# Kernel tuning notes

Hardware: AMD Instinct MI355X
Metric: run time of the kernel (lower is better)

Reference implementation:

```python
import jax, jax.numpy as jnp
import numpy as np
from jax import lax

EPS = 1e-5
IC = 32  # inter_channels

def bn(x, g, b, m, v):
    sh = (1, -1, 1, 1)
    return (x - m.reshape(sh)) * (g.reshape(sh) * lax.rsqrt(v.reshape(sh) + EPS)) + b.reshape(sh)

def prelu(x, a):
    return jnp.where(x >= 0, x, a * x)

def conv1x1(x, w):  # x: [B,C,H,W], w: [O,C]
    return jnp.einsum('bchw,oc->bohw', x, w)

def dconv(x, w, d):  # 3x3 dilated conv, same padding
    return lax.conv_general_dilated(x, w, (1, 1), [(d, d), (d, d)], rhs_dilation=(d, d),
                                    dimension_numbers=('NCHW', 'OIHW', 'NCHW'))

def glca_forward(feature, q_w, q_gamma, q_beta, q_mean, q_var, q_alpha,
                 k_w, k_gamma, k_beta, k_mean, k_var, k_alpha,
                 v_w, v_gamma, v_beta, v_mean, v_var, v_alpha,
                 d1_w, d1_gamma, d1_beta, d1_mean, d1_var,
                 d2_w, d2_gamma, d2_beta, d2_mean, d2_var,
                 d3_w, d3_gamma, d3_beta, d3_mean, d3_var,
                 o_w, o_gamma, o_beta, o_mean, o_var, o_alpha):
    B, C, H, W = feature.shape
    q = prelu(bn(conv1x1(feature, q_w), q_gamma, q_beta, q_mean, q_var), q_alpha)  # [B,IC,H,W]
    k = prelu(bn(conv1x1(feature, k_w), k_gamma, k_beta, k_mean, k_var), k_alpha)
    val = prelu(bn(conv1x1(feature, v_w), v_gamma, v_beta, v_mean, v_var), v_alpha)
    qr = q.transpose(0, 3, 2, 1).reshape(B * W, H, IC)   # [BW,H,IC]
    kr = k.transpose(0, 3, 1, 2).reshape(B * W, IC, H)   # [BW,IC,H]
    att = jax.nn.softmax(jnp.matmul(qr, kr), axis=-1)    # [BW,H,H]
    branches = []
    for w, g, b, m, var, d in ((d1_w, d1_gamma, d1_beta, d1_mean, d1_var, 1),
                               (d2_w, d2_gamma, d2_beta, d2_mean, d2_var, 3),
                               (d3_w, d3_gamma, d3_beta, d3_mean, d3_var, 5)):
        t = jax.nn.relu(bn(dconv(val, w, d), g, b, m, var))          # [B,IC,H,W]
        # faithful to source: permute(0,3,1,2) then raw view to [BW,H,IC]
        t = t.transpose(0, 3, 1, 2).reshape(B * W, H, IC)
        branches.append(jnp.matmul(att, t))                          # [BW,H,IC]
    # faithful to source: cat along dim 0, then raw view(B,W,H,-1)
    res = jnp.concatenate(branches, axis=0).reshape(B, W, H, 3 * IC)
    res = res.transpose(0, 3, 2, 1)                                  # [B,3*IC,H,W]
    out = prelu(bn(conv1x1(res, o_w), o_gamma, o_beta, o_mean, o_var) + feature, o_alpha)
    return out

def setup_inputs() -> dict:
    B, C, H, W = 8, 256, 160, 160
    key = jax.random.key(0)
    ks = iter(jax.random.split(key, 48))
    d = {}
    d['feature'] = jax.random.normal(next(ks), (B, C, H, W), jnp.float32)
    for p in ('q', 'k', 'v'):
        d[p + '_w'] = jax.random.normal(next(ks), (IC, C), jnp.float32) * 0.05
        d[p + '_gamma'] = jax.random.uniform(next(ks), (IC,), jnp.float32, 0.5, 1.5)
        d[p + '_beta'] = jax.random.normal(next(ks), (IC,), jnp.float32) * 0.1
        d[p + '_mean'] = jax.random.normal(next(ks), (IC,), jnp.float32) * 0.1
        d[p + '_var'] = jax.random.uniform(next(ks), (IC,), jnp.float32, 0.5, 1.5)
        d[p + '_alpha'] = jnp.full((1,), 0.25, jnp.float32)
    for p in ('d1', 'd2', 'd3'):
        d[p + '_w'] = jax.random.normal(next(ks), (IC, IC, 3, 3), jnp.float32) * 0.05
        d[p + '_gamma'] = jax.random.uniform(next(ks), (IC,), jnp.float32, 0.5, 1.5)
        d[p + '_beta'] = jax.random.normal(next(ks), (IC,), jnp.float32) * 0.1
        d[p + '_mean'] = jax.random.normal(next(ks), (IC,), jnp.float32) * 0.1
        d[p + '_var'] = jax.random.uniform(next(ks), (IC,), jnp.float32, 0.5, 1.5)
    d['o_w'] = jax.random.normal(next(ks), (C, 3 * IC), jnp.float32) * 0.05
    d['o_gamma'] = jax.random.uniform(next(ks), (C,), jnp.float32, 0.5, 1.5)
    d['o_beta'] = jax.random.normal(next(ks), (C,), jnp.float32) * 0.1
    d['o_mean'] = jax.random.normal(next(ks), (C,), jnp.float32) * 0.1
    d['o_var'] = jax.random.uniform(next(ks), (C,), jnp.float32, 0.5, 1.5)
    d['o_alpha'] = jnp.full((1,), 0.25, jnp.float32)
    return d

def reference(feature, q_w, q_gamma, q_beta, q_mean, q_var, q_alpha,
              k_w, k_gamma, k_beta, k_mean, k_var, k_alpha,
              v_w, v_gamma, v_beta, v_mean, v_var, v_alpha,
              d1_w, d1_gamma, d1_beta, d1_mean, d1_var,
              d2_w, d2_gamma, d2_beta, d2_mean, d2_var,
              d3_w, d3_gamma, d3_beta, d3_mean, d3_var,
              o_w, o_gamma, o_beta, o_mean, o_var, o_alpha):
    return glca_forward(feature, q_w, q_gamma, q_beta, q_mean, q_var, q_alpha,
                        k_w, k_gamma, k_beta, k_mean, k_var, k_alpha,
                        v_w, v_gamma, v_beta, v_mean, v_var, v_alpha,
                        d1_w, d1_gamma, d1_beta, d1_mean, d1_var,
                        d2_w, d2_gamma, d2_beta, d2_mean, d2_var,
                        d3_w, d3_gamma, d3_beta, d3_mean, d3_var,
                        o_w, o_gamma, o_beta, o_mean, o_var, o_alpha)
```

## Files before the change

kernel.cpp:

```cpp
#include <hip/hip_runtime.h>

constexpr int Hh = 160, Ww = 160, Bb = 8, Cc = 256, ICn = 32;
constexpr int HWn = Hh * Ww;
constexpr float EPSf = 1e-5f;

constexpr int P_WQH  = 0;
constexpr int P_WQL  = 12288;
constexpr int P_QKVB = 24576;
constexpr int P_QKVA = 24672;
constexpr int P_DWB  = 24768;
constexpr int P_DB   = 52416;
constexpr int P_OWB  = 52512;
constexpr int P_OB   = 77088;
constexpr int P_OA   = 77344;
constexpr int PLANE  = Bb * ICn * HWn;
constexpr int OFF_Q  = 77824;
constexpr int OFF_K  = OFF_Q + PLANE;
constexpr int OFF_V  = OFF_Q + 2 * PLANE;
constexpr int OFF_T  = OFF_Q + 3 * PLANE;
constexpr int OFF_TPF= OFF_T + (3 * PLANE) / 2;
constexpr int OFF_CAT= OFF_Q + 6 * PLANE;

typedef unsigned short u16;
typedef short bf16x8 __attribute__((ext_vector_type(8)));
typedef float f32x4  __attribute__((ext_vector_type(4)));

__device__ __forceinline__ unsigned f2b(float x) {
    unsigned u = __float_as_uint(x);
    return (u + 0x7FFFu + ((u >> 16) & 1u)) >> 16;
}
__device__ __forceinline__ float b2f(unsigned b) { return __uint_as_float(b << 16); }

struct InPtrs { const float* p[40]; };

__global__ void k_prep(InPtrs in, float* __restrict__ ws) {
    int idx = blockIdx.x * 256 + threadIdx.x;
    if (idx < 24576) {
        int oc = idx >> 8, c = idx & 255;
        int z = oc >> 5, o = oc & 31;
        const float* wz = in.p[1 + 6 * z];
        float s = in.p[2 + 6 * z][o] * rsqrtf(in.p[5 + 6 * z][o] + EPSf);
        float wf = wz[o * 256 + c] * s;
        unsigned hi = f2b(wf);
        unsigned lo = f2b(wf - b2f(hi));
        ((u16*)(ws + P_WQH))[oc * 256 + c] = (u16)hi;
        ((u16*)(ws + P_WQL))[oc * 256 + c] = (u16)lo;
    } else if (idx < 24672) {
        int oc = idx - 24576; int z = oc >> 5, o = oc & 31;
        float s = in.p[2 + 6 * z][o] * rsqrtf(in.p[5 + 6 * z][o] + EPSf);
        ws[P_QKVB + oc] = in.p[3 + 6 * z][o] - in.p[4 + 6 * z][o] * s;
    } else if (idx < 24768) {
        int oc = idx - 24672; int z = oc >> 5;
        ws[P_QKVA + oc] = in.p[6 + 6 * z][0];
    } else if (idx < 52416) {
        int j = idx - 24768;
        int d = j / 9216, r2 = j % 9216;
        int oc = r2 & 31; int tmp = r2 >> 5;
        int kx = tmp % 3; tmp /= 3; int ky = tmp % 3; int ic2 = tmp / 3;
        const float* wd = in.p[19 + 5 * d];
        float s = in.p[20 + 5 * d][oc] * rsqrtf(in.p[23 + 5 * d][oc] + EPSf);
        float wf = wd[((oc * 32 + ic2) * 3 + ky) * 3 + kx] * s;
        ((u16*)(ws + P_DWB))[((d * 9 + ky * 3 + kx) * 32 + oc) * 32 + ic2] = (u16)f2b(wf);
    } else if (idx < 52512) {
        int j = idx - 52416; int d = j >> 5, oc = j & 31;
        float s = in.p[20 + 5 * d][oc] * rsqrtf(in.p[23 + 5 * d][oc] + EPSf);
        ws[P_DB + j] = in.p[21 + 5 * d][oc] - in.p[22 + 5 * d][oc] * s;
    } else if (idx < 77088) {
        int j2 = idx - 52512; int c = j2 / 96;
        float s = in.p[35][c] * rsqrtf(in.p[38][c] + EPSf);
        ((u16*)(ws + P_OWB))[j2] = (u16)f2b(in.p[34][j2] * s);
    } else if (idx < 77344) {
        int c = idx - 77088;
        float s = in.p[35][c] * rsqrtf(in.p[38][c] + EPSf);
        ws[P_OB + c] = in.p[36][c] - in.p[37][c] * s;
    } else if (idx == 77344) {
        ws[P_OA] = in.p[39][0];
    }
}

__global__ __launch_bounds__(64) void k_vpad(float* __restrict__ ws) {
    u16* Vt = (u16*)(ws + OFF_V);
    size_t base = (size_t)blockIdx.x * 176 * 32;
    int t = threadIdx.x;
    int off = (t < 32) ? t * 8 : (168 * 32 + (t - 32) * 8);
    uint4 z = {0u, 0u, 0u, 0u};
    *(uint4*)(Vt + base + off) = z;
}

__global__ __launch_bounds__(256) void k_qkv(const float* __restrict__ feat,
                                             float* __restrict__ ws) {
    __shared__ float FS[64 * 132];
    const int tid = threadIdx.x;
    const int wv = tid >> 6, l = tid & 63;
    const int g = l >> 4, c15 = l & 15;
    const int n0 = blockIdx.x * 128;
    const int b = n0 / HWn, hw0 = n0 % HWn;
    const float* fbase = feat + (size_t)b * Cc * HWn + hw0;
    const u16* __restrict__ WQH = (const u16*)(ws + P_WQH);
    const u16* __restrict__ WQL = (const u16*)(ws + P_WQL);

    f32x4 acc[6][2];
    f32x4 z4 = {0.f, 0.f, 0.f, 0.f};
#pragma unroll
    for (int mt = 0; mt < 6; mt++) { acc[mt][0] = z4; acc[mt][1] = z4; }

    for (int kc = 0; kc < 4; kc++) {
        __syncthreads();
#pragma unroll
        for (int i = 0; i < 8; i++) {
            int f = tid + i * 256;
            int row = f >> 5, col4 = f & 31;
            float4 v = *(const float4*)(fbase + (size_t)(kc * 64 + row) * HWn + col4 * 4);
            *(float4*)(&FS[row * 132 + col4 * 4]) = v;
        }
        __syncthreads();
#pragma unroll
        for (int ks = 0; ks < 2; ks++) {
            bf16x8 bh[2], bl[2];
#pragma unroll
            for (int ntl = 0; ntl < 2; ntl++) {
                int pos = (wv * 2 + ntl) * 16 + c15;
                unsigned hw_[4], lw_[4];
#pragma unroll
                for (int v2 = 0; v2 < 4; v2++) {
                    float x0 = FS[(ks * 32 + g * 8 + 2 * v2) * 132 + pos];
                    float x1 = FS[(ks * 32 + g * 8 + 2 * v2 + 1) * 132 + pos];
                    unsigned h0 = f2b(x0), h1 = f2b(x1);
                    unsigned l0 = f2b(x0 - b2f(h0)), l1 = f2b(x1 - b2f(h1));
                    hw_[v2] = h0 | (h1 << 16);
                    lw_[v2] = l0 | (l1 << 16);
                }
                uint4 hv = {hw_[0], hw_[1], hw_[2], hw_[3]};
                uint4 lv = {lw_[0], lw_[1], lw_[2], lw_[3]};
                bh[ntl] = *(bf16x8*)&hv;
                bl[ntl] = *(bf16x8*)&lv;
            }
#pragma unroll
            for (int mt = 0; mt < 6; mt++) {
                int arow = (16 * mt + c15) * 256 + kc * 64 + ks * 32 + g * 8;
                bf16x8 ah = *(const bf16x8*)(WQH + arow);
                bf16x8 al = *(const bf16x8*)(WQL + arow);
#pragma unroll
                for (int ntl = 0; ntl < 2; ntl++) {
                    acc[mt][ntl] = __builtin_amdgcn_mfma_f32_16x16x32_bf16(ah, bh[ntl], acc[mt][ntl], 0, 0, 0);
                    acc[mt][ntl] = __builtin_amdgcn_mfma_f32_16x16x32_bf16(ah, bl[ntl], acc[mt][ntl], 0, 0, 0);
                    acc[mt][ntl] = __builtin_amdgcn_mfma_f32_16x16x32_bf16(al, bh[ntl], acc[mt][ntl], 0, 0, 0);
                }
            }
        }
    }

    u16* vt = (u16*)(ws + OFF_V);
#pragma unroll
    for (int mt = 0; mt < 6; mt++)
#pragma unroll
        for (int ntl = 0; ntl < 2; ntl++) {
            int pos = hw0 + (wv * 2 + ntl) * 16 + c15;
            if (mt < 4) {
#pragma unroll
                for (int jr = 0; jr < 4; jr++) {
                    int oc = 16 * mt + 4 * g + jr;
                    float bb = ws[P_QKVB + oc];
                    float aa = ws[P_QKVA + oc];
                    float y = acc[mt][ntl][jr] + bb;
                    y = y >= 0.f ? y : aa * y;
                    int z = oc >> 5, o = oc & 31;
                    ws[OFF_Q + (size_t)z * PLANE + ((size_t)b * ICn + o) * HWn + pos] = y;
                }
            } else {
                int h = pos / 160, w2 = pos % 160;
                unsigned r[2];
#pragma unroll
                for (int p = 0; p < 2; p++) {
                    int oc = 16 * mt + 4 * g + 2 * p;
                    float y0 = acc[mt][ntl][2 * p]     + ws[P_QKVB + oc];
                    float y1 = acc[mt][ntl][2 * p + 1] + ws[P_QKVB + oc + 1];
                    float a0 = ws[P_QKVA + oc], a1 = ws[P_QKVA + oc + 1];
                    y0 = y0 >= 0.f ? y0 : a0 * y0;
                    y1 = y1 >= 0.f ? y1 : a1 * y1;
                    r[p] = f2b(y0) | (f2b(y1) << 16);
                }
                size_t a = ((size_t)(b * 160 + h) * 176 + w2 + 8) * 32 + (mt - 4) * 16 + 4 * g;
                uint2 dd; dd.x = r[0]; dd.y = r[1];
                *(uint2*)(vt + a) = dd;
            }
        }
}

__global__ __launch_bounds__(256) void k_dconv(float* __restrict__ ws) {
    const int tid = threadIdx.x;
    const int wv = tid >> 6, l = tid & 63;
    const int g = l >> 4, c15 = l & 15;
    const int b = blockIdx.y;
    const int d = blockIdx.z;
    const int dil = 1 + 2 * d;
    const int h0 = blockIdx.x * 2;
    const u16* __restrict__ WB = (const u16*)(ws + P_DWB) + d * 9 * 32 * 32;
    bf16x8 wb[9][2];
#pragma unroll
    for (int tap = 0; tap < 9; tap++)
#pragma unroll
        for (int n = 0; n < 2; n++)
            wb[tap][n] = *(const bf16x8*)(WB + ((size_t)tap * 32 + n * 16 + c15) * 32 + g * 8);
    const u16* __restrict__ Vt = (const u16*)(ws + OFF_V) + (size_t)b * 160 * 176 * 32;
    const float bias0 = ws[P_DB + d * 32 + c15];
    const float bias1 = ws[P_DB + d * 32 + 16 + c15];
    u16* __restrict__ tp = (u16*)(ws + OFF_TPF) + (size_t)(d * Bb + b) * ICn * HWn;
    f32x4 z4 = {0.f, 0.f, 0.f, 0.f};

    for (int t5 = 0; t5 < 5; t5++) {
        int t = wv * 5 + t5;
        int h = h0 + (t >= 10);
        int w0 = (t % 10) * 16;
        f32x4 acc0 = z4, acc1 = z4;
#pragma unroll
        for (int ky = 0; ky < 3; ky++) {
            int hh = h + dil * (ky - 1);
            if ((unsigned)hh >= 160u) continue;
            const u16* row = Vt + (size_t)hh * 176 * 32;
#pragma unroll
            for (int kx = 0; kx < 3; kx++) {
                int wbase = w0 + dil * (kx - 1) + 8;
                bf16x8 av = *(const bf16x8*)(row + (size_t)(wbase + c15) * 32 + g * 8);
                acc0 = __builtin_amdgcn_mfma_f32_16x16x32_bf16(av, wb[ky * 3 + kx][0], acc0, 0, 0, 0);
                acc1 = __builtin_amdgcn_mfma_f32_16x16x32_bf16(av, wb[ky * 3 + kx][1], acc1, 0, 0, 0);
            }
        }
        size_t pixb = (size_t)h * 160 + w0 + 4 * g;
        uint2 o0, o1;
        o0.x = f2b(fmaxf(acc0[0] + bias0, 0.f)) | (f2b(fmaxf(acc0[1] + bias0, 0.f)) << 16);
        o0.y = f2b(fmaxf(acc0[2] + bias0, 0.f)) | (f2b(fmaxf(acc0[3] + bias0, 0.f)) << 16);
        o1.x = f2b(fmaxf(acc1[0] + bias1, 0.f)) | (f2b(fmaxf(acc1[1] + bias1, 0.f)) << 16);
        o1.y = f2b(fmaxf(acc1[2] + bias1, 0.f)) | (f2b(fmaxf(acc1[3] + bias1, 0.f)) << 16);
        *(uint2*)(tp + (size_t)c15 * HWn + pixb) = o0;
        *(uint2*)(tp + (size_t)(16 + c15) * HWn + pixb) = o1;
    }
}

__global__ __launch_bounds__(256) void k_tfrag(float* __restrict__ ws) {
    __shared__ u16 fr[4][5120];
    const int tid = threadIdx.x;
    const int wq = blockIdx.x;
    const int b  = blockIdx.y;
    const int d  = blockIdx.z;
    const int w0 = wq * 4;
    const u16* __restrict__ tp = (const u16*)(ws + OFF_TPF) + (size_t)(d * Bb + b) * ICn * HWn;
    for (int i = tid; i < 5120; i += 256) {
        int ic = i / 160, h = i % 160;
        uint2 v = *(const uint2*)(tp + (size_t)ic * HWn + h * Ww + w0);
        fr[0][i] = (u16)(v.x & 0xFFFFu);
        fr[1][i] = (u16)(v.x >> 16);
        fr[2][i] = (u16)(v.y & 0xFFFFu);
        fr[3][i] = (u16)(v.y >> 16);
    }
    __syncthreads();
    u16* __restrict__ tf = (u16*)(ws + OFF_T);
#pragma unroll
    for (int it = 0; it < 10; it++) {
        int W = tid + it * 256;
        int s = W / 640, word = W % 640;
        int slot = word >> 6, lane = word & 63;
        int jc = (lane & 15) | ((slot / 5) << 4);
        int h2b = ((slot % 5) << 5) | (((lane >> 4) & 3) << 3);
        unsigned r[4];
#pragma unroll
        for (int p = 0; p < 4; p++) {
            int f0 = (h2b + 2 * p) * 32 + jc;
            unsigned lo = fr[s][f0];
            unsigned hi = fr[s][f0 + 32];
            r[p] = lo | (hi << 16);
        }
        uint4 o4 = {r[0], r[1], r[2], r[3]};
        *(uint4*)(tf + ((size_t)d * 1280 + b * 160 + w0 + s) * 5120 + word * 8) = o4;
    }
}

__device__ __forceinline__ void stage_qk_hilo(const float* __restrict__ g,
                                              char* hi_buf, char* lo_buf, int tid) {
#pragma unroll
    for (int ss = 0; ss < 2; ss++) {
        int s = tid + ss * 320;
        int l = s & 63, rt = s >> 6;
        int h = 16 * rt + (l & 15);
        int icb = (l >> 4) * 8;
        const float* gp = g + (size_t)icb * HWn + h * Ww;
        unsigned hb[8], lb[8];
#pragma unroll
        for (int v = 0; v < 8; v++) {
            float x = gp[(size_t)v * HWn];
            hb[v] = f2b(x);
            lb[v] = f2b(x - b2f(hb[v]));
        }
        uint4 hv = {hb[0] | (hb[1] << 16), hb[2] | (hb[3] << 16),
                    hb[4] | (hb[5] << 16), hb[6] | (hb[7] << 16)};
        uint4 lv = {lb[0] | (lb[1] << 16), lb[2] | (lb[3] << 16),
                    lb[4] | (lb[5] << 16), lb[6] | (lb[7] << 16)};
        *(uint4*)(hi_buf + s * 16) = hv;
        *(uint4*)(lo_buf + s * 16) = lv;
    }
}

__global__ __launch_bounds__(320) void k_att(float* __restrict__ ws) {
    extern __shared__ char smem[];
    char* q_hi = smem;
    char* q_lo = smem + 10240;
    char* k_hi = smem + 20480;
    char* k_lo = smem + 30720;
    char* Sb   = smem;
    const int tid = threadIdx.x;
    const int bid = blockIdx.x;
    const int r8 = bid & 7, qq = bid >> 3;
    const int b = qq / 20;
    const int w = r8 * 20 + (qq % 20);
    const int bw = b * Ww + w;
    const int wv = tid >> 6;
    const int l  = tid & 63;
    const int g  = l >> 4;
    const int c  = l & 15;

    const float* qg = ws + OFF_Q + (size_t)b * ICn * HWn + w;
    const float* kg = ws + OFF_K + (size_t)b * ICn * HWn + w;
    stage_qk_hilo(qg, q_hi, q_lo, tid);
    stage_qk_hilo(kg, k_hi, k_lo, tid);
    __syncthreads();

    bf16x8 bq[2][2];
#pragma unroll
    for (int ct = 0; ct < 2; ct++) {
        int tau = 2 * wv + ct;
        bq[ct][0] = *(bf16x8*)(q_hi + (tau * 64 + l) * 16);
        bq[ct][1] = *(bf16x8*)(q_lo + (tau * 64 + l) * 16);
    }
    f32x4 acc[10][2];
    f32x4 z4 = {0.f, 0.f, 0.f, 0.f};
#pragma unroll
    for (int rt = 0; rt < 10; rt++) { acc[rt][0] = z4; acc[rt][1] = z4; }
#pragma unroll
    for (int rt = 0; rt < 10; rt++) {
        bf16x8 ah = *(bf16x8*)(k_hi + (rt * 64 + l) * 16);
        bf16x8 al = *(bf16x8*)(k_lo + (rt * 64 + l) * 16);
#pragma unroll
        for (int ct = 0; ct < 2; ct++) {
            acc[rt][ct] = __builtin_amdgcn_mfma_f32_16x16x32_bf16(ah, bq[ct][0], acc[rt][ct], 0, 0, 0);
            acc[rt][ct] = __builtin_amdgcn_mfma_f32_16x16x32_bf16(ah, bq[ct][1], acc[rt][ct], 0, 0, 0);
            acc[rt][ct] = __builtin_amdgcn_mfma_f32_16x16x32_bf16(al, bq[ct][0], acc[rt][ct], 0, 0, 0);
        }
    }
    __syncthreads();

    float mx[2] = {-3.4e38f, -3.4e38f};
#pragma unroll
    for (int rt = 0; rt < 10; rt++)
#pragma unroll
        for (int ct = 0; ct < 2; ct++)
#pragma unroll
            for (int j = 0; j < 4; j++) mx[ct] = fmaxf(mx[ct], acc[rt][ct][j]);
#pragma unroll
    for (int ct = 0; ct < 2; ct++) {
        mx[ct] = fmaxf(mx[ct], __shfl_xor(mx[ct], 16));
        mx[ct] = fmaxf(mx[ct], __shfl_xor(mx[ct], 32));
    }
    float sm[2] = {0.f, 0.f};
#pragma unroll
    for (int rt = 0; rt < 10; rt++)
#pragma unroll
        for (int ct = 0; ct < 2; ct++)
#pragma unroll
            for (int j = 0; j < 4; j++) {
                float e = __expf(acc[rt][ct][j] - mx[ct]);
                acc[rt][ct][j] = e;
                sm[ct] += e;
            }
#pragma unroll
    for (int ct = 0; ct < 2; ct++) {
        sm[ct] += __shfl_xor(sm[ct], 16);
        sm[ct] += __shfl_xor(sm[ct], 32);
    }
    float inv[2] = {1.f / sm[0], 1.f / sm[1]};

#pragma unroll
    for (int rt = 0; rt < 10; rt++) {
#pragma unroll
        for (int ct = 0; ct < 2; ct++) {
            float p0 = acc[rt][ct][0] * inv[ct];
            float p1 = acc[rt][ct][1] * inv[ct];
            float p2 = acc[rt][ct][2] * inv[ct];
            float p3 = acc[rt][ct][3] * inv[ct];
            unsigned d0 = f2b(p0) | (f2b(p1) << 16);
            unsigned d1 = f2b(p2) | (f2b(p3) << 16);
            int Lf = c + 16 * (2 * (rt & 1) + (g >> 1));
            char* dst = Sb + (((wv * 2 + ct) * 5 + (rt >> 1)) * 64 + Lf) * 16 + 8 * (g & 1);
            uint2 dd; dd.x = d0; dd.y = d1;
            *(uint2*)dst = dd;
        }
    }
    __syncthreads();

    const u16* tf = (const u16*)(ws + OFF_T);
    u16* catb = (u16*)(ws + OFF_CAT);
    for (int d = 0; d < 3; d++) {
        const u16* tfd = tf + ((size_t)d * (Bb * Ww) + bw) * 5120;
        f32x4 po[2][2];
        po[0][0] = z4; po[0][1] = z4; po[1][0] = z4; po[1][1] = z4;
#pragma unroll
        for (int ks = 0; ks < 5; ks++) {
            bf16x8 a0 = *(const bf16x8*)(tfd + ((0 * 5 + ks) * 64 + l) * 8);
            bf16x8 a1 = *(const bf16x8*)(tfd + ((1 * 5 + ks) * 64 + l) * 8);
            bf16x8 s0 = *(bf16x8*)(Sb + (((wv * 2 + 0) * 5 + ks) * 64 + l) * 16);
            bf16x8 s1 = *(bf16x8*)(Sb + (((wv * 2 + 1) * 5 + ks) * 64 + l) * 16);
            po[0][0] = __builtin_amdgcn_mfma_f32_16x16x32_bf16(a0, s0, po[0][0], 0, 0, 0);
            po[0][1] = __builtin_amdgcn_mfma_f32_16x16x32_bf16(a0, s1, po[0][1], 0, 0, 0);
            po[1][0] = __builtin_amdgcn_mfma_f32_16x16x32_bf16(a1, s0, po[1][0], 0, 0, 0);
            po[1][1] = __builtin_amdgcn_mfma_f32_16x16x32_bf16(a1, s1, po[1][1], 0, 0, 0);
        }
#pragma unroll
        for (int jt = 0; jt < 2; jt++)
#pragma unroll
            for (int ct = 0; ct < 2; ct++) {
                int h1 = 32 * wv + 16 * ct + c;
                size_t idx = (size_t)d * PLANE + (size_t)bw * 5120 + h1 * 32 + 16 * jt + 4 * g;
                f32x4 v = po[jt][ct];
                uint2 dd;
                dd.x = f2b(v[0]) | (f2b(v[1]) << 16);
                dd.y = f2b(v[2]) | (f2b(v[3]) << 16);
                *(uint2*)(catb + idx) = dd;
            }
    }
}

__global__ __launch_bounds__(256) void k_out(const float* __restrict__ feat,
                                             const float* __restrict__ ws,
                                             float* __restrict__ out) {
    __shared__ u16 Bs[12288];
    const int tid = threadIdx.x;
    const int wv = tid >> 6, l = tid & 63;
    const int g = l >> 4, c15 = l & 15;
    const int n0 = blockIdx.x * 128;
    const int b = n0 / HWn, hw0 = n0 % HWn;
    const u16* __restrict__ CATb = (const u16*)(ws + OFF_CAT);
    const u16* __restrict__ OWB = (const u16*)(ws + P_OWB);

#pragma unroll
    for (int ss = 0; ss < 6; ss++) {
        int s = tid + ss * 256;
        int sl = s & 63, si = s >> 6;
        int p = (si & 7) * 16 + (sl & 15);
        int hw = hw0 + p;
        int h = hw / Ww, w2 = hw % Ww;
        int j = (si >> 3) * 32 + (sl >> 4) * 8;
        size_t flat = ((size_t)(b * Ww + w2) * Hh + h) * 96 + j;
        *(uint4*)(&Bs[(si * 64 + sl) * 8]) = *(const uint4*)(CATb + flat);
    }
    bf16x8 af[4][3];
#pragma unroll
    for (int mt = 0; mt < 4; mt++)
#pragma unroll
        for (int ks = 0; ks < 3; ks++)
            af[mt][ks] = *(const bf16x8*)(OWB + (wv * 64 + mt * 16 + c15) * 96 + ks * 32 + g * 8);
    __syncthreads();
    const float alpha = ws[P_OA];

    f32x4 z4 = {0.f, 0.f, 0.f, 0.f};
#pragma unroll
    for (int np = 0; np < 2; np++) {
        f32x4 acc[4][4];
#pragma unroll
        for (int mt = 0; mt < 4; mt++)
#pragma unroll
            for (int ntl = 0; ntl < 4; ntl++) acc[mt][ntl] = z4;
#pragma unroll
        for (int ks = 0; ks < 3; ks++) {
            bf16x8 bf_[4];
#pragma unroll
            for (int ntl = 0; ntl < 4; ntl++)
                bf_[ntl] = *(const bf16x8*)(&Bs[((ks * 8 + np * 4 + ntl) * 64 + l) * 8]);
#pragma unroll
            for (int mt = 0; mt < 4; mt++)
#pragma unroll
                for (int ntl = 0; ntl < 4; ntl++)
                    acc[mt][ntl] = __builtin_amdgcn_mfma_f32_16x16x32_bf16(af[mt][ks], bf_[ntl], acc[mt][ntl], 0, 0, 0);
        }
#pragma unroll
        for (int mt = 0; mt < 4; mt++)
#pragma unroll
            for (int ntl = 0; ntl < 4; ntl++) {
                int p = (np * 4 + ntl) * 16 + c15;
#pragma unroll
                for (int jr = 0; jr < 4; jr++) {
                    int cch = wv * 64 + mt * 16 + 4 * g + jr;
                    size_t base = ((size_t)b * Cc + cch) * HWn + hw0 + p;
                    float y = acc[mt][ntl][jr] + ws[P_OB + cch] + feat[base];
                    out[base] = y >= 0.f ? y : alpha * y;
                }
            }
    }
}

extern "C" void kernel_launch(void* const* d_in, const int* in_sizes, int n_in,
                              void* d_out, int out_size, void* d_ws, size_t ws_size,
                              hipStream_t stream) {
    InPtrs ip;
    for (int i = 0; i < 40; i++) ip.p[i] = (const float*)d_in[i];
    float* ws = (float*)d_ws;
    const float* feat = (const float*)d_in[0];
    float* out = (float*)d_out;

    k_prep<<<304, 256, 0, stream>>>(ip, ws);
    k_vpad<<<1280, 64, 0, stream>>>(ws);
    k_qkv<<<1600, 256, 0, stream>>>(feat, ws);
    k_dconv<<<dim3(80, 8, 3), 256, 0, stream>>>(ws);
    k_tfrag<<<dim3(40, 8, 3), 256, 0, stream>>>(ws);
    (void)hipFuncSetAttribute(reinterpret_cast<const void*>(k_att),
                              hipFuncAttributeMaxDynamicSharedMemorySize, 51200);
    k_att<<<1280, 320, 51200, stream>>>(ws);
    k_out<<<1600, 256, 0, stream>>>(feat, ws, out);
}
```

Baseline: 466.7 us.

## Precompute Q/K hi-lo bf16 MFMA fragments in a separate coalesced kernel

Adds k_qkfrag, which reads Q and K for four w columns at once with float4 loads and transposes them through shared memory. It splits each value into hi and lo bf16 parts in MFMA fragment order and writes them to free workspace regions (the V and TPF areas). k_att then loads these fragments straight from global memory instead of gathering strided fp32 columns, and drops two barriers and its dynamic shared memory. The aim is to replace the uncoalesced column gather in the attention kernel. The cost is an extra launch and an extra round trip of the fragment data through global memory, and it relies on the V plane no longer being needed at that point.

```diff
diff --git a/kernel.cpp b/kernel.cpp
--- a/kernel.cpp
+++ b/kernel.cpp
@@ -275,38 +275,52 @@
     }
 }
 
-__device__ __forceinline__ void stage_qk_hilo(const float* __restrict__ g,
-                                              char* hi_buf, char* lo_buf, int tid) {
-#pragma unroll
-    for (int ss = 0; ss < 2; ss++) {
-        int s = tid + ss * 320;
-        int l = s & 63, rt = s >> 6;
-        int h = 16 * rt + (l & 15);
-        int icb = (l >> 4) * 8;
-        const float* gp = g + (size_t)icb * HWn + h * Ww;
-        unsigned hb[8], lb[8];
-#pragma unroll
-        for (int v = 0; v < 8; v++) {
-            float x = gp[(size_t)v * HWn];
-            hb[v] = f2b(x);
-            lb[v] = f2b(x - b2f(hb[v]));
-        }
-        uint4 hv = {hb[0] | (hb[1] << 16), hb[2] | (hb[3] << 16),
-                    hb[4] | (hb[5] << 16), hb[6] | (hb[7] << 16)};
-        uint4 lv = {lb[0] | (lb[1] << 16), lb[2] | (lb[3] << 16),
-                    lb[4] | (lb[5] << 16), lb[6] | (lb[7] << 16)};
-        *(uint4*)(hi_buf + s * 16) = hv;
-        *(uint4*)(lo_buf + s * 16) = lv;
+__global__ __launch_bounds__(256) void k_qkfrag(float* __restrict__ ws) {
+    extern __shared__ float frf[];
+    const int tid = threadIdx.x;
+    const int wq = blockIdx.x;
+    const int b  = blockIdx.y;
+    const int z  = blockIdx.z;
+    const int w0 = wq * 4;
+    const float* __restrict__ in = ws + (z ? OFF_K : OFF_Q) + (size_t)b * ICn * HWn;
+    u16* __restrict__ outb = (u16*)(ws + (z ? OFF_TPF : OFF_V));
+
+    for (int i = tid; i < 5120; i += 256) {
+        int ic = i / 160, h = i % 160;
+        float4 v = *(const float4*)(in + (size_t)ic * HWn + h * 160 + w0);
+        frf[0 * 5120 + i] = v.x;
+        frf[1 * 5120 + i] = v.y;
+        frf[2 * 5120 + i] = v.z;
+        frf[3 * 5120 + i] = v.w;
+    }
+    __syncthreads();
+#pragma unroll
+    for (int it = 0; it < 10; it++) {
+        int W = tid + it * 256;
+        int s = W / 640, word = W % 640;
+        int lane = word & 63, tau = word >> 6;
+        int h = tau * 16 + (lane & 15);
+        int icb = (lane >> 4) * 8;
+        unsigned hw_[4], lw_[4];
+#pragma unroll
+        for (int p = 0; p < 4; p++) {
+            float x0 = frf[s * 5120 + (icb + 2 * p) * 160 + h];
+            float x1 = frf[s * 5120 + (icb + 2 * p + 1) * 160 + h];
+            unsigned h0 = f2b(x0), h1 = f2b(x1);
+            unsigned l0 = f2b(x0 - b2f(h0)), l1 = f2b(x1 - b2f(h1));
+            hw_[p] = h0 | (h1 << 16);
+            lw_[p] = l0 | (l1 << 16);
+        }
+        uint4 hv = {hw_[0], hw_[1], hw_[2], hw_[3]};
+        uint4 lv = {lw_[0], lw_[1], lw_[2], lw_[3]};
+        size_t o = (size_t)(b * 160 + w0 + s) * 5120 + word * 8;
+        *(uint4*)(outb + o) = hv;
+        *(uint4*)(outb + (size_t)PLANE + o) = lv;
     }
 }
 
 __global__ __launch_bounds__(320) void k_att(float* __restrict__ ws) {
-    extern __shared__ char smem[];
-    char* q_hi = smem;
-    char* q_lo = smem + 10240;
-    char* k_hi = smem + 20480;
-    char* k_lo = smem + 30720;
-    char* Sb   = smem;
+    __shared__ char Sb[51200];
     const int tid = threadIdx.x;
     const int bid = blockIdx.x;
     const int r8 = bid & 7, qq = bid >> 3;
@@ -317,19 +331,19 @@
     const int l  = tid & 63;
     const int g  = l >> 4;
     const int c  = l & 15;
-
-    const float* qg = ws + OFF_Q + (size_t)b * ICn * HWn + w;
-    const float* kg = ws + OFF_K + (size_t)b * ICn * HWn + w;
-    stage_qk_hilo(qg, q_hi, q_lo, tid);
-    stage_qk_hilo(kg, k_hi, k_lo, tid);
-    __syncthreads();
+    const int slice = b * 160 + w;
+
+    const u16* __restrict__ qh = (const u16*)(ws + OFF_V)   + (size_t)slice * 5120;
+    const u16* __restrict__ ql = qh + (size_t)PLANE;
+    const u16* __restrict__ kh = (const u16*)(ws + OFF_TPF) + (size_t)slice * 5120;
+    const u16* __restrict__ kl = kh + (size_t)PLANE;
 
     bf16x8 bq[2][2];
 #pragma unroll
     for (int ct = 0; ct < 2; ct++) {
         int tau = 2 * wv + ct;
-        bq[ct][0] = *(bf16x8*)(q_hi + (tau * 64 + l) * 16);
-        bq[ct][1] = *(bf16x8*)(q_lo + (tau * 64 + l) * 16);
+        bq[ct][0] = *(const bf16x8*)(qh + (tau * 64 + l) * 8);
+        bq[ct][1] = *(const bf16x8*)(ql + (tau * 64 + l) * 8);
     }
     f32x4 acc[10][2];
     f32x4 z4 = {0.f, 0.f, 0.f, 0.f};
@@ -337,8 +351,8 @@
     for (int rt = 0; rt < 10; rt++) { acc[rt][0] = z4; acc[rt][1] = z4; }
 #pragma unroll
     for (int rt = 0; rt < 10; rt++) {
-        bf16x8 ah = *(bf16x8*)(k_hi + (rt * 64 + l) * 16);
-        bf16x8 al = *(bf16x8*)(k_lo + (rt * 64 + l) * 16);
+        bf16x8 ah = *(const bf16x8*)(kh + (rt * 64 + l) * 8);
+        bf16x8 al = *(const bf16x8*)(kl + (rt * 64 + l) * 8);
 #pragma unroll
         for (int ct = 0; ct < 2; ct++) {
             acc[rt][ct] = __builtin_amdgcn_mfma_f32_16x16x32_bf16(ah, bq[ct][0], acc[rt][ct], 0, 0, 0);
@@ -346,7 +360,6 @@
             acc[rt][ct] = __builtin_amdgcn_mfma_f32_16x16x32_bf16(al, bq[ct][0], acc[rt][ct], 0, 0, 0);
         }
     }
-    __syncthreads();
 
     float mx[2] = {-3.4e38f, -3.4e38f};
 #pragma unroll
@@ -394,7 +407,6 @@
             *(uint2*)dst = dd;
         }
     }
-    __syncthreads();
 
     const u16* tf = (const u16*)(ws + OFF_T);
     u16* catb = (u16*)(ws + OFF_CAT);
@@ -510,8 +522,9 @@
     k_qkv<<<1600, 256, 0, stream>>>(feat, ws);
     k_dconv<<<dim3(80, 8, 3), 256, 0, stream>>>(ws);
     k_tfrag<<<dim3(40, 8, 3), 256, 0, stream>>>(ws);
-    (void)hipFuncSetAttribute(reinterpret_cast<const void*>(k_att),
-                              hipFuncAttributeMaxDynamicSharedMemorySize, 51200);
-    k_att<<<1280, 320, 51200, stream>>>(ws);
+    (void)hipFuncSetAttribute(reinterpret_cast<const void*>(k_qkfrag),
+                              hipFuncAttributeMaxDynamicSharedMemorySize, 81920);
+    k_qkfrag<<<dim3(40, 8, 2), 256, 81920, stream>>>(ws);
+    k_att<<<1280, 320, 0, stream>>>(ws);
     k_out<<<1600, 256, 0, stream>>>(feat, ws, out);
 }
```

Measured after the change: 471.2 us. No clear change (+1.0%).
